# Performance work log

Hardware: AMD Instinct MI355X
Metric: run time of the kernel (lower is better)

## Reference

```python
import jax, jax.numpy as jnp
import numpy as np

C, B, D = 1_000_000, 4096, 128

def setup_inputs() -> dict:
    key = jax.random.key(0)
    ks = jax.random.split(key, 7)
    nodes = jax.random.normal(ks[0], (C, D), dtype=jnp.float32)
    z_local = jax.random.normal(ks[1], (B, D), dtype=jnp.float32)
    z_meta = jax.random.normal(ks[2], (D,), dtype=jnp.float32)
    # MLP params: Linear(3D -> D), GELU, Linear(D -> 1)
    W1 = jax.random.normal(ks[3], (3 * D, D), dtype=jnp.float32) / np.sqrt(3 * D)
    b1 = jnp.zeros((D,), dtype=jnp.float32)
    W2 = jax.random.normal(ks[4], (D, 1), dtype=jnp.float32) / np.sqrt(D)
    b2 = jnp.zeros((1,), dtype=jnp.float32)
    batch = jnp.sort(jax.random.randint(ks[5], (C,), 0, B, dtype=jnp.int64))
    return {"nodes": nodes, "z_local": z_local, "z_meta": z_meta,
            "W1": W1, "b1": b1, "W2": W2, "b2": b2, "batch": batch}

def reference(nodes, z_local, z_meta, W1, b1, W2, b2, batch):
    # gather per-graph global vector for each node, broadcast batch-wide meta
    z_local_tiled = z_local[batch]                       # [C, D]
    z_meta_tiled = jnp.broadcast_to(z_meta[None, :], nodes.shape)  # [C, D]
    combined = jnp.concatenate([nodes, z_local_tiled, z_meta_tiled], axis=-1)  # [C, 3D]
    h = jax.nn.gelu(combined @ W1 + b1, approximate=False)  # [C, D]
    logits = (h @ W2 + b2).squeeze(-1)                       # [C]
    return logits
```

## Files before the change

### kernel.cpp

```cpp
#include <hip/hip_runtime.h>
#include <hip/hip_bf16.h>
#include <cstdint>


typedef __attribute__((ext_vector_type(8))) __bf16 bf16x8;
typedef __attribute__((ext_vector_type(4))) float f32x4;
typedef __attribute__((address_space(3))) uint32_t lds_u32;
typedef __attribute__((address_space(1))) const uint32_t glob_u32;

#define D_DIM 128

__device__ __forceinline__ float gelu_exact(float x) {
    float t = 0.70710678118654752f * x;
    float a = fabsf(t);
    float d = __builtin_amdgcn_rcpf(fmaf(0.3275911f, a, 1.0f));
    float p = fmaf(1.061405429f, d, -1.453152027f);
    p = fmaf(p, d, 1.421413741f);
    p = fmaf(p, d, -0.284496736f);
    p = fmaf(p, d, 0.254829592f);
    p = p * d;
    float e = __builtin_amdgcn_exp2f(a * a * -1.4426950408889634f);
    float erf_a = fmaf(-p, e, 1.0f);
    float erf_t = copysignf(erf_a, t);
    return 0.5f * x * (1.0f + erf_t);
}

__global__ __launch_bounds__(256) void prep_all(
    const float* __restrict__ z_local, const float* __restrict__ z_meta,
    const float* __restrict__ W1, const float* __restrict__ b1,
    __bf16* __restrict__ w1f, float* __restrict__ bias2, float* __restrict__ pre) {
    const int blk = blockIdx.x;
    const int tid = threadIdx.x;
    if (blk < 64) {
        int f = blk * 256 + tid;
        int j = f & 7, lane = (f >> 3) & 63, nt = (f >> 9) & 7, kc = f >> 12;
        int k = kc * 32 + (lane >> 4) * 8 + j;
        int n = nt * 16 + (lane & 15);
        w1f[f] = (__bf16)W1[k * D_DIM + n];
    } else if (blk == 64) {
        if (tid < D_DIM) {
            int n = tid;
            float s = b1[n];
            for (int k = 0; k < D_DIM; ++k)
                s = fmaf(z_meta[k], W1[(2 * D_DIM + k) * D_DIM + n], s);
            bias2[n] = s;
        }
    } else {
        int pb = blk - 65;
        int n = tid & 127;
        int g0 = pb * 8 + (tid >> 7) * 4;
        float s[4] = {0.f, 0.f, 0.f, 0.f};
        for (int k = 0; k < D_DIM; ++k) {
            float wk = W1[(D_DIM + k) * D_DIM + n];
#pragma unroll
            for (int g = 0; g < 4; ++g)
                s[g] = fmaf(z_local[(size_t)(g0 + g) * D_DIM + k], wk, s[g]);
        }
#pragma unroll
        for (int g = 0; g < 4; ++g) pre[(size_t)(g0 + g) * D_DIM + n] = s[g];
    }
}

__global__ __launch_bounds__(256) void readout_main(
    const float* __restrict__ nodes, const int* __restrict__ batch,
    const float* __restrict__ pre, const __bf16* __restrict__ w1f,
    const float* __restrict__ bias2, const float* __restrict__ W2,
    const float* __restrict__ b2, float* __restrict__ out) {
    __shared__ __bf16 w1s[16384];
    const int tid = threadIdx.x;
    const int wave = tid >> 6;
    const int lane = tid & 63;
    const int q = lane >> 4;
    const int c0 = lane & 15;
    const int row_base = blockIdx.x * 64 + wave * 16;

    const float* aptr = nodes + (size_t)(row_base + c0) * D_DIM + q * 8;
    f32x4 a[8];
#pragma unroll
    for (int kc = 0; kc < 4; ++kc) {
        a[2 * kc]     = *((const f32x4*)(aptr + kc * 32));
        a[2 * kc + 1] = *((const f32x4*)(aptr + kc * 32 + 4));
    }

    {
        const __bf16* gsrc = w1f + wave * 4096;
        __bf16* ldst = w1s + wave * 4096;
#pragma unroll
        for (int it = 0; it < 8; ++it) {
            __builtin_amdgcn_global_load_lds(
                (glob_u32*)(gsrc + it * 512 + lane * 8),
                (lds_u32*)(ldst + it * 512), 16, 0, 0);
        }
    }

    int brow[4];
#pragma unroll
    for (int r = 0; r < 4; ++r) brow[r] = batch[row_base + q * 4 + r];
    float w2v[8], bz[8];
#pragma unroll
    for (int nt = 0; nt < 8; ++nt) {
        w2v[nt] = W2[nt * 16 + c0];
        bz[nt]  = bias2[nt * 16 + c0];
    }
    const float b2v = b2[0];

    __syncthreads();

    f32x4 acc[8] = {};
    const bf16x8* bfr = (const bf16x8*)w1s;
#pragma unroll
    for (int kc = 0; kc < 4; ++kc) {
        bf16x8 af;
#pragma unroll
        for (int j = 0; j < 8; ++j)
            af[j] = (__bf16)a[2 * kc + (j >> 2)][j & 3];
#pragma unroll
        for (int nt = 0; nt < 8; ++nt) {
            bf16x8 bf = bfr[(kc * 8 + nt) * 64 + lane];
            acc[nt] = __builtin_amdgcn_mfma_f32_16x16x32_bf16(af, bf, acc[nt], 0, 0, 0);
        }
    }

#pragma unroll
    for (int r = 0; r < 4; ++r) {
        const float* prow = pre + (size_t)brow[r] * D_DIM;
        float partial = 0.f;
#pragma unroll
        for (int nt = 0; nt < 8; ++nt) {
            float u = acc[nt][r] + prow[nt * 16 + c0] + bz[nt];
            partial += gelu_exact(u) * w2v[nt];
        }
        partial += __shfl_xor(partial, 1);
        partial += __shfl_xor(partial, 2);
        partial += __shfl_xor(partial, 4);
        partial += __shfl_xor(partial, 8);
        if (c0 == 0) out[row_base + q * 4 + r] = partial + b2v;
    }
}

extern "C" void kernel_launch(void* const* d_in, const int* in_sizes, int n_in,
                              void* d_out, int out_size, void* d_ws, size_t ws_size,
                              hipStream_t stream) {
    const float* nodes   = (const float*)d_in[0];
    const float* z_local = (const float*)d_in[1];
    const float* z_meta  = (const float*)d_in[2];
    const float* W1      = (const float*)d_in[3];
    const float* b1      = (const float*)d_in[4];
    const float* W2      = (const float*)d_in[5];
    const float* b2      = (const float*)d_in[6];
    const int*   batch   = (const int*)d_in[7];
    float* out = (float*)d_out;

    char* ws = (char*)d_ws;
    __bf16* w1f  = (__bf16*)ws;
    float* bias2 = (float*)(ws + 32768);
    float* pre   = (float*)(ws + 33280);

    prep_all<<<577, 256, 0, stream>>>(z_local, z_meta, W1, b1, w1f, bias2, pre);
    readout_main<<<15625, 256, 0, stream>>>(nodes, batch, pre, w1f, bias2, W2, b2, out);
}
```

Before: 690.3 us.

## Make readout persistent with double-buffered node tiles and fold meta bias into pre

The main kernel becomes a persistent grid of 512 blocks. Each wave walks over 16-row strips with a stride and prefetches the next strip's node rows and batch ids into a second register buffer while it computes the current strip. The W1 fragment is loaded into LDS once per block instead of once per 64 rows. The prep kernel now folds the z_meta·W1 bias into the per-graph pre table, stages z_local and z_meta in shared memory, and uses more blocks. This removes a per-element bias add and a bias2 buffer. Register pressure rises because two tiles are held at once, and fewer blocks may limit how much latency the hardware can hide.

Result: slower. 752.4 us (+9.0%).

```diff
diff --git a/kernel.cpp b/kernel.cpp
--- a/kernel.cpp
+++ b/kernel.cpp
@@ -9,6 +9,10 @@
 typedef __attribute__((address_space(1))) const uint32_t glob_u32;
 
 #define D_DIM 128
+#define NROWS 1000000
+#define NSTRIPS (NROWS / 16)
+#define MAIN_GRID 512
+#define WAVES_TOTAL (MAIN_GRID * 4)
 
 __device__ __forceinline__ float gelu_exact(float x) {
     float t = 0.70710678118654752f * x;
@@ -28,7 +32,7 @@
 __global__ __launch_bounds__(256) void prep_all(
     const float* __restrict__ z_local, const float* __restrict__ z_meta,
     const float* __restrict__ W1, const float* __restrict__ b1,
-    __bf16* __restrict__ w1f, float* __restrict__ bias2, float* __restrict__ pre) {
+    __bf16* __restrict__ w1f, float* __restrict__ pre) {
     const int blk = blockIdx.x;
     const int tid = threadIdx.x;
     if (blk < 64) {
@@ -37,50 +41,46 @@
         int k = kc * 32 + (lane >> 4) * 8 + j;
         int n = nt * 16 + (lane & 15);
         w1f[f] = (__bf16)W1[k * D_DIM + n];
-    } else if (blk == 64) {
-        if (tid < D_DIM) {
-            int n = tid;
-            float s = b1[n];
-            for (int k = 0; k < D_DIM; ++k)
-                s = fmaf(z_meta[k], W1[(2 * D_DIM + k) * D_DIM + n], s);
-            bias2[n] = s;
+    } else {
+        __shared__ float zl[4][D_DIM];
+        __shared__ float zm[D_DIM];
+        const int pb = blk - 64;
+        const int n = tid & 127;
+        const int half = tid >> 7;
+        for (int i = tid; i < 4 * D_DIM; i += 256)
+            zl[i >> 7][i & 127] =
+                z_local[(size_t)(pb * 4 + (i >> 7)) * D_DIM + (i & 127)];
+        if (tid < D_DIM) zm[tid] = z_meta[tid];
+        __syncthreads();
+
+        float s0 = 0.f, s1 = 0.f, sm = b1[n];
+        const float* wmid = W1 + (size_t)D_DIM * D_DIM + n;
+        const float* whi  = W1 + (size_t)2 * D_DIM * D_DIM + n;
+#pragma unroll 8
+        for (int k = 0; k < D_DIM; ++k) {
+            float wm = wmid[k * D_DIM];
+            float wh = whi[k * D_DIM];
+            s0 = fmaf(zl[half * 2][k],     wm, s0);
+            s1 = fmaf(zl[half * 2 + 1][k], wm, s1);
+            sm = fmaf(zm[k],               wh, sm);
         }
-    } else {
-        int pb = blk - 65;
-        int n = tid & 127;
-        int g0 = pb * 8 + (tid >> 7) * 4;
-        float s[4] = {0.f, 0.f, 0.f, 0.f};
-        for (int k = 0; k < D_DIM; ++k) {
-            float wk = W1[(D_DIM + k) * D_DIM + n];
-#pragma unroll
-            for (int g = 0; g < 4; ++g)
-                s[g] = fmaf(z_local[(size_t)(g0 + g) * D_DIM + k], wk, s[g]);
-        }
-#pragma unroll
-        for (int g = 0; g < 4; ++g) pre[(size_t)(g0 + g) * D_DIM + n] = s[g];
+        const int g0 = pb * 4 + half * 2;
+        pre[(size_t)g0 * D_DIM + n]       = s0 + sm;
+        pre[(size_t)(g0 + 1) * D_DIM + n] = s1 + sm;
     }
 }
 
 __global__ __launch_bounds__(256) void readout_main(
     const float* __restrict__ nodes, const int* __restrict__ batch,
     const float* __restrict__ pre, const __bf16* __restrict__ w1f,
-    const float* __restrict__ bias2, const float* __restrict__ W2,
-    const float* __restrict__ b2, float* __restrict__ out) {
+    const float* __restrict__ W2, const float* __restrict__ b2,
+    float* __restrict__ out) {
     __shared__ __bf16 w1s[16384];
     const int tid = threadIdx.x;
     const int wave = tid >> 6;
     const int lane = tid & 63;
     const int q = lane >> 4;
     const int c0 = lane & 15;
-    const int row_base = blockIdx.x * 64 + wave * 16;
-
-    const float* aptr = nodes + (size_t)(row_base + c0) * D_DIM + q * 8;
-    f32x4 a[8];
-#pragma unroll
-    for (int kc = 0; kc < 4; ++kc) {
-        a[2 * kc]     = *((const f32x4*)(aptr + kc * 32));
-        a[2 * kc + 1] = *((const f32x4*)(aptr + kc * 32 + 4));
-    }
 
     {
         const __bf16* gsrc = w1f + wave * 4096;
@@ -93,48 +93,72 @@
         }
     }
 
-    int brow[4];
+    float w2v[8];
 #pragma unroll
-    for (int r = 0; r < 4; ++r) brow[r] = batch[row_base + q * 4 + r];
-    float w2v[8], bz[8];
-#pragma unroll
-    for (int nt = 0; nt < 8; ++nt) {
-        w2v[nt] = W2[nt * 16 + c0];
-        bz[nt]  = bias2[nt * 16 + c0];
-    }
+    for (int nt = 0; nt < 8; ++nt) w2v[nt] = W2[nt * 16 + c0];
     const float b2v = b2[0];
 
+    const int wgid = blockIdx.x * 4 + wave;
+
+    auto load_tile = [&](f32x4* a, int* br, int s) {
+        const float* aptr = nodes + (size_t)(s * 16 + c0) * D_DIM + q * 8;
+#pragma unroll
+        for (int kc = 0; kc < 4; ++kc) {
+            a[2 * kc]     = *((const f32x4*)(aptr + kc * 32));
+            a[2 * kc + 1] = *((const f32x4*)(aptr + kc * 32 + 4));
+        }
+#pragma unroll
+        for (int r = 0; r < 4; ++r) br[r] = batch[s * 16 + q * 4 + r];
+    };
+
+    auto compute_tile = [&](const f32x4* a, const int* br, int s) {
+        f32x4 acc[8] = {};
+        const bf16x8* bfr = (const bf16x8*)w1s;
+#pragma unroll
+        for (int kc = 0; kc < 4; ++kc) {
+            bf16x8 af;
+#pragma unroll
+            for (int j = 0; j < 8; ++j)
+                af[j] = (__bf16)a[2 * kc + (j >> 2)][j & 3];
+#pragma unroll
+            for (int nt = 0; nt < 8; ++nt) {
+                bf16x8 bf = bfr[(kc * 8 + nt) * 64 + lane];
+                acc[nt] = __builtin_amdgcn_mfma_f32_16x16x32_bf16(af, bf, acc[nt], 0, 0, 0);
+            }
+        }
+#pragma unroll
+        for (int r = 0; r < 4; ++r) {
+            const float* prow = pre + (size_t)br[r] * D_DIM;
+            float partial = 0.f;
+#pragma unroll
+            for (int nt = 0; nt < 8; ++nt) {
+                float u = acc[nt][r] + prow[nt * 16 + c0];
+                partial += gelu_exact(u) * w2v[nt];
+            }
+            partial += __shfl_xor(partial, 1);
+            partial += __shfl_xor(partial, 2);
+            partial += __shfl_xor(partial, 4);
+            partial += __shfl_xor(partial, 8);
+            if (c0 == 0) out[s * 16 + q * 4 + r] = partial + b2v;
+        }
+    };
+
+    f32x4 aA[8], aB[8];
+    int brA[4], brB[4];
+    int sA = wgid;
+    load_tile(aA, brA, sA);
     __syncthreads();
 
-    f32x4 acc[8] = {};
-    const bf16x8* bfr = (const bf16x8*)w1s;
-#pragma unroll
-    for (int kc = 0; kc < 4; ++kc) {
-        bf16x8 af;
-#pragma unroll
-        for (int j = 0; j < 8; ++j)
-            af[j] = (__bf16)a[2 * kc + (j >> 2)][j & 3];
-#pragma unroll
-        for (int nt = 0; nt < 8; ++nt) {
-            bf16x8 bf = bfr[(kc * 8 + nt) * 64 + lane];
-            acc[nt] = __builtin_amdgcn_mfma_f32_16x16x32_bf16(af, bf, acc[nt], 0, 0, 0);
-        }
-    }
-
-#pragma unroll
-    for (int r = 0; r < 4; ++r) {
-        const float* prow = pre + (size_t)brow[r] * D_DIM;
-        float partial = 0.f;
-#pragma unroll
-        for (int nt = 0; nt < 8; ++nt) {
-            float u = acc[nt][r] + prow[nt * 16 + c0] + bz[nt];
-            partial += gelu_exact(u) * w2v[nt];
-        }
-        partial += __shfl_xor(partial, 1);
-        partial += __shfl_xor(partial, 2);
-        partial += __shfl_xor(partial, 4);
-        partial += __shfl_xor(partial, 8);
-        if (c0 == 0) out[row_base + q * 4 + r] = partial + b2v;
+    while (true) {
+        int sB = sA + WAVES_TOTAL;
+        load_tile(aB, brB, sB < NSTRIPS ? sB : wgid);
+        compute_tile(aA, brA, sA);
+        if (sB >= NSTRIPS) break;
+        int sC = sB + WAVES_TOTAL;
+        load_tile(aA, brA, sC < NSTRIPS ? sC : wgid);
+        compute_tile(aB, brB, sB);
+        if (sC >= NSTRIPS) break;
+        sA = sC;
     }
 }
 
@@ -152,10 +176,9 @@
     float* out = (float*)d_out;
 
     char* ws = (char*)d_ws;
-    __bf16* w1f  = (__bf16*)ws;
-    float* bias2 = (float*)(ws + 32768);
-    float* pre   = (float*)(ws + 33280);
+    __bf16* w1f = (__bf16*)ws;
+    float* pre  = (float*)(ws + 32768);
 
-    prep_all<<<577, 256, 0, stream>>>(z_local, z_meta, W1, b1, w1f, bias2, pre);
-    readout_main<<<15625, 256, 0, stream>>>(nodes, batch, pre, w1f, bias2, W2, b2, out);
+    prep_all<<<1088, 256, 0, stream>>>(z_local, z_meta, W1, b1, w1f, pre);
+    readout_main<<<MAIN_GRID, 256, 0, stream>>>(nodes, batch, pre, w1f, W2, b2, out);
 }
```

## Process two 64-row tiles per block to amortize W1 LDS staging

Applied to the files above, without the earlier changes.

Each block now handles 128 rows instead of 64, reusing the staged W1 fragments in LDS for two MFMA passes and halving the grid. The second tile's node loads and batch indices are issued before the first tile's compute, and the gathered pre rows are prefetched into registers ahead of the epilogue, to overlap memory latency. This costs extra registers (two A tiles plus the prefetched pre values), which may lower occupancy. The last block skips the second tile because the row count is not a multiple of 128.

Result: no change. 690.6 us (+0.0%).

```diff
diff --git a/kernel.cpp b/kernel.cpp
--- a/kernel.cpp
+++ b/kernel.cpp
@@ -9,6 +9,7 @@
 typedef __attribute__((address_space(1))) const uint32_t glob_u32;
 
 #define D_DIM 128
+#define NROWS 1000000
 
 __device__ __forceinline__ float gelu_exact(float x) {
     float t = 0.70710678118654752f * x;
@@ -72,15 +73,20 @@
     const int lane = tid & 63;
     const int q = lane >> 4;
     const int c0 = lane & 15;
-    const int row_base = blockIdx.x * 64 + wave * 16;
-
-    const float* aptr = nodes + (size_t)(row_base + c0) * D_DIM + q * 8;
-    f32x4 a[8];
+    const int row1 = blockIdx.x * 128 + wave * 16;
+    const int row2 = row1 + 64;
+    const bool has2 = (blockIdx.x < (NROWS / 128));
+
+    const float* aptr1 = nodes + (size_t)(row1 + c0) * D_DIM + q * 8;
+    f32x4 a1[8];
 #pragma unroll
     for (int kc = 0; kc < 4; ++kc) {
-        a[2 * kc]     = *((const f32x4*)(aptr + kc * 32));
-        a[2 * kc + 1] = *((const f32x4*)(aptr + kc * 32 + 4));
-    }
+        a1[2 * kc]     = *((const f32x4*)(aptr1 + kc * 32));
+        a1[2 * kc + 1] = *((const f32x4*)(aptr1 + kc * 32 + 4));
+    }
+    int br1[4];
+#pragma unroll
+    for (int r = 0; r < 4; ++r) br1[r] = batch[row1 + q * 4 + r];
 
     {
         const __bf16* gsrc = w1f + wave * 4096;
@@ -93,9 +99,6 @@
         }
     }
 
-    int brow[4];
-#pragma unroll
-    for (int r = 0; r < 4; ++r) brow[r] = batch[row_base + q * 4 + r];
     float w2v[8], bz[8];
 #pragma unroll
     for (int nt = 0; nt < 8; ++nt) {
@@ -106,35 +109,93 @@
 
     __syncthreads();
 
+    float p1[4][8];
+#pragma unroll
+    for (int r = 0; r < 4; ++r) {
+        const float* prow = pre + (size_t)br1[r] * D_DIM;
+#pragma unroll
+        for (int nt = 0; nt < 8; ++nt) p1[r][nt] = prow[nt * 16 + c0];
+    }
+
+    f32x4 a2[8];
+    int br2[4];
+    if (has2) {
+        const float* aptr2 = nodes + (size_t)(row2 + c0) * D_DIM + q * 8;
+#pragma unroll
+        for (int kc = 0; kc < 4; ++kc) {
+            a2[2 * kc]     = *((const f32x4*)(aptr2 + kc * 32));
+            a2[2 * kc + 1] = *((const f32x4*)(aptr2 + kc * 32 + 4));
+        }
+#pragma unroll
+        for (int r = 0; r < 4; ++r) br2[r] = batch[row2 + q * 4 + r];
+    }
+
+    const bf16x8* bfr = (const bf16x8*)w1s;
+
     f32x4 acc[8] = {};
-    const bf16x8* bfr = (const bf16x8*)w1s;
 #pragma unroll
     for (int kc = 0; kc < 4; ++kc) {
         bf16x8 af;
 #pragma unroll
         for (int j = 0; j < 8; ++j)
-            af[j] = (__bf16)a[2 * kc + (j >> 2)][j & 3];
+            af[j] = (__bf16)a1[2 * kc + (j >> 2)][j & 3];
 #pragma unroll
         for (int nt = 0; nt < 8; ++nt) {
             bf16x8 bf = bfr[(kc * 8 + nt) * 64 + lane];
             acc[nt] = __builtin_amdgcn_mfma_f32_16x16x32_bf16(af, bf, acc[nt], 0, 0, 0);
         }
     }
-
-#pragma unroll
-    for (int r = 0; r < 4; ++r) {
-        const float* prow = pre + (size_t)brow[r] * D_DIM;
+#pragma unroll
+    for (int r = 0; r < 4; ++r) {
         float partial = 0.f;
 #pragma unroll
         for (int nt = 0; nt < 8; ++nt) {
-            float u = acc[nt][r] + prow[nt * 16 + c0] + bz[nt];
+            float u = acc[nt][r] + p1[r][nt] + bz[nt];
             partial += gelu_exact(u) * w2v[nt];
         }
         partial += __shfl_xor(partial, 1);
         partial += __shfl_xor(partial, 2);
         partial += __shfl_xor(partial, 4);
         partial += __shfl_xor(partial, 8);
-        if (c0 == 0) out[row_base + q * 4 + r] = partial + b2v;
+        if (c0 == 0) out[row1 + q * 4 + r] = partial + b2v;
+    }
+
+    if (!has2) return;
+
+#pragma unroll
+    for (int r = 0; r < 4; ++r) {
+        const float* prow = pre + (size_t)br2[r] * D_DIM;
+#pragma unroll
+        for (int nt = 0; nt < 8; ++nt) p1[r][nt] = prow[nt * 16 + c0];
+    }
+
+#pragma unroll
+    for (int nt = 0; nt < 8; ++nt) acc[nt] = (f32x4){0.f, 0.f, 0.f, 0.f};
+#pragma unroll
+    for (int kc = 0; kc < 4; ++kc) {
+        bf16x8 af;
+#pragma unroll
+        for (int j = 0; j < 8; ++j)
+            af[j] = (__bf16)a2[2 * kc + (j >> 2)][j & 3];
+#pragma unroll
+        for (int nt = 0; nt < 8; ++nt) {
+            bf16x8 bf = bfr[(kc * 8 + nt) * 64 + lane];
+            acc[nt] = __builtin_amdgcn_mfma_f32_16x16x32_bf16(af, bf, acc[nt], 0, 0, 0);
+        }
+    }
+#pragma unroll
+    for (int r = 0; r < 4; ++r) {
+        float partial = 0.f;
+#pragma unroll
+        for (int nt = 0; nt < 8; ++nt) {
+            float u = acc[nt][r] + p1[r][nt] + bz[nt];
+            partial += gelu_exact(u) * w2v[nt];
+        }
+        partial += __shfl_xor(partial, 1);
+        partial += __shfl_xor(partial, 2);
+        partial += __shfl_xor(partial, 4);
+        partial += __shfl_xor(partial, 8);
+        if (c0 == 0) out[row2 + q * 4 + r] = partial + b2v;
     }
 }
 
@@ -157,5 +218,5 @@
     float* pre   = (float*)(ws + 33280);
 
     prep_all<<<577, 256, 0, stream>>>(z_local, z_meta, W1, b1, w1f, bias2, pre);
-    readout_main<<<15625, 256, 0, stream>>>(nodes, batch, pre, w1f, bias2, W2, b2, out);
-}
+    readout_main<<<7813, 256, 0, stream>>>(nodes, batch, pre, w1f, bias2, W2, b2, out);
+}
```
